# Optimization experiments

Measured on AMD Instinct MI355X. Metric: run time of the kernel, lower is better.

The kernel has to match this reference:

```python
import jax, jax.numpy as jnp
import numpy as np
from jax import lax

TAG_NUM = 20
START = TAG_NUM - 2  # tag2idx[START_TAG]
STOP = TAG_NUM - 1   # tag2idx[STOP_TAG]
NEG = -10000.0


def setup_inputs() -> dict:
    key = jax.random.key(0)
    k1, k2, k3, k4 = jax.random.split(key, 4)
    B, L = 256, 512
    feats = jax.random.normal(k1, (B, L, TAG_NUM), dtype=jnp.float32)
    T = jax.random.normal(k2, (TAG_NUM, TAG_NUM), dtype=jnp.float32)
    # transitions into START and out of... match torch init: T[START, :] = -1e4 ; T[:, STOP] = -1e4
    T = T.at[START, :].set(NEG).at[:, STOP].set(NEG)
    tags = jax.random.randint(k3, (B, L), 0, TAG_NUM - 2, dtype=jnp.int64)  # real tags only
    lengths = jax.random.randint(k4, (B,), 1, L + 1, dtype=jnp.int64)
    return {"feats": feats, "T": T, "tags": tags, "lengths": lengths}


def crf_neg_log_likelihood(feats, T, tags, lengths):
    # feats: [B, L, tag], T: [tag, tag] (T[i, j] = score of transition i -> j)
    B, L, tg = feats.shape
    mask = jnp.arange(L)[None, :] < lengths[:, None]           # [B, L] bool
    # scores[b, l, prev, cur] = feats[b, l, cur] + T[prev, cur]
    scores = feats[:, :, None, :] + T[None, None, :, :]        # [B, L, tag, tag]
    scores_lb = jnp.swapaxes(scores, 0, 1)                     # [L, B, tag, tag]
    mask_lb = mask.T                                           # [L, B]

    # ---- forward algorithm (log partition) ----
    part0 = scores_lb[0, :, START, :]                          # [B, tag]
    def step(part, x):
        sc, m = x                                              # sc: [B, tag, tag], m: [B]
        cur = jax.nn.logsumexp(sc + part[:, :, None], axis=1)  # [B, tag]
        part = jnp.where(m[:, None], cur, part)                # freeze past seq end
        return part, None
    part, _ = lax.scan(step, part0, (scores_lb[1:], mask_lb[1:]))
    final = jax.nn.logsumexp(part[:, :, None] + T[None, :, :], axis=1)  # [B, tag]
    forward_score = final[:, STOP].sum()

    # ---- gold score ----
    prev = jnp.concatenate([jnp.full((B, 1), START, dtype=tags.dtype), tags[:, :-1]], axis=1)
    b_idx = jnp.arange(B)[:, None]
    l_idx = jnp.arange(L)[None, :]
    tg_energy = scores[b_idx, l_idx, prev, tags]               # [B, L]
    gold = jnp.sum(tg_energy * mask.astype(feats.dtype))
    end_ids = jnp.take_along_axis(tags, lengths[:, None] - 1, axis=1)[:, 0]
    gold = gold + T[end_ids, STOP].sum()

    return forward_score - gold


def reference(feats, T, tags, lengths):
    return crf_neg_log_likelihood(feats, T, tags, lengths)
```

## Files before the change

### kernel.cpp

```cpp
#include <hip/hip_runtime.h>
#include <hip/hip_bf16.h>
#include <math.h>

#define TAGS   20
#define TSTART (TAGS - 2)
#define TSTOP  (TAGS - 1)

constexpr float  LOG2E = 1.4426950408889634f;
constexpr float  LN2f  = 0.6931471805599453f;
constexpr double LN2d  = 0.69314718055994530942;

typedef __attribute__((ext_vector_type(8))) short short8;
typedef __attribute__((ext_vector_type(4))) float f32x4;
union U4 { unsigned int u[4]; short8 v; };

__device__ __forceinline__ unsigned int pk2(float lo, float hi) {
    unsigned int a = __float_as_uint(hi) + 0x8000u;
    unsigned int b = __float_as_uint(lo) + 0x8000u;
#if __has_builtin(__builtin_amdgcn_perm)
    return __builtin_amdgcn_perm(a, b, 0x07060302u);
#else
    return (a & 0xFFFF0000u) | (b >> 16);
#endif
}
__device__ __forceinline__ float fexp2(float x) { return exp2f(x); }
__device__ __forceinline__ float flog2(float x) { return log2f(x); }
__device__ __forceinline__ float frcp(float x) { return __builtin_amdgcn_rcpf(x); }
__device__ __forceinline__ float bcast(float v, int srclane) {
    return __int_as_float(__builtin_amdgcn_readlane(__float_as_int(v), srclane));
}
__device__ __forceinline__ int rho(int k) {
    int g = k >> 3, i = k & 7;
    return (i < 4) ? (4 * g + i) : (16 + 4 * g + (i - 4));
}

__global__ __launch_bounds__(512)
void crf_fused_kernel(const float* __restrict__ feats,
                      const float* __restrict__ Tm,
                      const int*   __restrict__ tags,
                      const int*   __restrict__ lengths,
                      double*      __restrict__ partial,
                      int L)
{
    __shared__ float  smem[16 * 1024];
    __shared__ float  sv[32];
    __shared__ int    EsX[8];
    __shared__ float  gred[8];
    __shared__ double fwd_sh;

    const int b    = blockIdx.x;
    const int tid  = threadIdx.x;
    const int w    = tid >> 6;
    const int lane = tid & 63;
    const int G    = lane >> 4, col = lane & 15;
    const int len  = lengths[b];

    #pragma unroll
    for (int s = 0; s < 2; ++s) {
        const int c = w + 8 * s;
        float* efc = smem + c * 1024;
        const float* fc = feats + ((size_t)b * L + (size_t)c * 32) * TAGS;
        for (int it = lane; it < 160; it += 64) {
            float4 v = reinterpret_cast<const float4*>(fc)[it];
            float vv[4] = {v.x, v.y, v.z, v.w};
            #pragma unroll
            for (int u = 0; u < 4; ++u) {
                int f = it * 4 + u;
                int t = f / TAGS, tag = f - t * TAGS;
                efc[t * 32 + tag] = fexp2(vv[u] * LOG2E);
            }
        }
        for (int q = lane; q < 32 * 12; q += 64) {
            int t = q / 12;
            efc[t * 32 + 20 + (q - t * 12)] = 0.f;
        }
    }
    __syncthreads();

    U4 A0, A1;
    #pragma unroll
    for (int t = 0; t < 4; ++t) {
        int k0 = 8 * G + 2 * t;
        int r0 = rho(k0), r1 = rho(k0 + 1);
        int m1 = 16 + col;
        float a00 = (r0 < TAGS) ? fexp2(Tm[col * TAGS + r0] * LOG2E) : 0.f;
        float a01 = (r1 < TAGS) ? fexp2(Tm[col * TAGS + r1] * LOG2E) : 0.f;
        float a10 = (m1 < TAGS && r0 < TAGS) ? fexp2(Tm[m1 * TAGS + r0] * LOG2E) : 0.f;
        float a11 = (m1 < TAGS && r1 < TAGS) ? fexp2(Tm[m1 * TAGS + r1] * LOG2E) : 0.f;
        A0.u[t] = pk2(a00, a01);
        A1.u[t] = pk2(a10, a11);
    }

    auto step = [&](f32x4& C00, f32x4& C01, f32x4& C10, f32x4& C11,
                    const float* efc, int t) {
        float4 e0 = *reinterpret_cast<const float4*>(&efc[t * 32 + 4 * G]);
        float4 e1 = *reinterpret_cast<const float4*>(&efc[t * 32 + 16 + 4 * G]);
        U4 B0, B1;
        B0.u[0] = pk2(C00[0] * e0.x, C00[1] * e0.y);
        B0.u[1] = pk2(C00[2] * e0.z, C00[3] * e0.w);
        B0.u[2] = pk2(C10[0] * e1.x, C10[1] * e1.y);
        B0.u[3] = pk2(C10[2] * e1.z, C10[3] * e1.w);
        B1.u[0] = pk2(C01[0] * e0.x, C01[1] * e0.y);
        B1.u[1] = pk2(C01[2] * e0.z, C01[3] * e0.w);
        B1.u[2] = pk2(C11[0] * e1.x, C11[1] * e1.y);
        B1.u[3] = pk2(C11[2] * e1.z, C11[3] * e1.w);
        f32x4 z = {0.f, 0.f, 0.f, 0.f};
        C00 = __builtin_amdgcn_mfma_f32_16x16x32_bf16(A0.v, B0.v, z, 0, 0, 0);
        C01 = __builtin_amdgcn_mfma_f32_16x16x32_bf16(A0.v, B1.v, z, 0, 0, 0);
        C10 = __builtin_amdgcn_mfma_f32_16x16x32_bf16(A1.v, B0.v, z, 0, 0, 0);
        C11 = __builtin_amdgcn_mfma_f32_16x16x32_bf16(A1.v, B1.v, z, 0, 0, 0);
    };
    auto strip = [&](f32x4& C00, f32x4& C01, f32x4& C10, f32x4& C11) -> int {
        float pr = C00[0] + C00[1] + C00[2] + C00[3] + C10[0] + C10[1] + C10[2] + C10[3];
        int pb = __builtin_amdgcn_readfirstlane(__float_as_int(pr));
        int ex = ((pb >> 23) & 0xFF) - 127;
        float s = __uint_as_float((unsigned)(127 - ex) << 23);
        #pragma unroll
        for (int j = 0; j < 4; ++j) { C00[j] *= s; C01[j] *= s; C10[j] *= s; C11[j] *= s; }
        return ex;
    };
    auto xwr = [&](int slot, const f32x4& C00, const f32x4& C01,
                   const f32x4& C10, const f32x4& C11, int E) {
        float* Xs = smem + slot * 1088;
        #pragma unroll
        for (int j = 0; j < 4; ++j) {
            Xs[(4 * G + j) * 34 + col]           = C00[j];
            Xs[(4 * G + j) * 34 + col + 16]      = C01[j];
            Xs[(16 + 4 * G + j) * 34 + col]      = C10[j];
            Xs[(16 + 4 * G + j) * 34 + col + 16] = C11[j];
        }
        if (lane == 0) EsX[slot] = E;
    };
    auto prod = [&](int slot, f32x4& C00, f32x4& C01, f32x4& C10, f32x4& C11) -> int {
        const float* Xs = smem + slot * 1088;
        U4 Ax0, Ax1;
        #pragma unroll
        for (int t = 0; t < 4; ++t) {
            int r = rho(8 * G + 2 * t);
            float2 x0 = *reinterpret_cast<const float2*>(&Xs[col * 34 + r]);
            float2 x1 = *reinterpret_cast<const float2*>(&Xs[(16 + col) * 34 + r]);
            Ax0.u[t] = pk2(x0.x, x0.y);
            Ax1.u[t] = pk2(x1.x, x1.y);
        }
        U4 B0, B1;
        B0.u[0] = pk2(C00[0], C00[1]);
        B0.u[1] = pk2(C00[2], C00[3]);
        B0.u[2] = pk2(C10[0], C10[1]);
        B0.u[3] = pk2(C10[2], C10[3]);
        B1.u[0] = pk2(C01[0], C01[1]);
        B1.u[1] = pk2(C01[2], C01[3]);
        B1.u[2] = pk2(C11[0], C11[1]);
        B1.u[3] = pk2(C11[2], C11[3]);
        f32x4 z = {0.f, 0.f, 0.f, 0.f};
        f32x4 n00 = __builtin_amdgcn_mfma_f32_16x16x32_bf16(Ax0.v, B0.v, z, 0, 0, 0);
        f32x4 n01 = __builtin_amdgcn_mfma_f32_16x16x32_bf16(Ax0.v, B1.v, z, 0, 0, 0);
        f32x4 n10 = __builtin_amdgcn_mfma_f32_16x16x32_bf16(Ax1.v, B0.v, z, 0, 0, 0);
        f32x4 n11 = __builtin_amdgcn_mfma_f32_16x16x32_bf16(Ax1.v, B1.v, z, 0, 0, 0);
        C00 = n00; C01 = n01; C10 = n10; C11 = n11;
        return strip(C00, C01, C10, C11);
    };

    f32x4 aC00, aC01, aC10, aC11, bC00, bC01, bC10, bC11;
    #pragma unroll
    for (int j = 0; j < 4; ++j) {
        float d = (4 * G + j == col) ? 1.f : 0.f;
        aC00[j] = d; aC11[j] = d; aC01[j] = 0.f; aC10[j] = 0.f;
        bC00[j] = d; bC11[j] = d; bC01[j] = 0.f; bC10[j] = 0.f;
    }
    int aE = 0, bE = 0;

    const int cB  = w + 8;
    const int loA = (w == 0) ? 1 : w * 32;
    const int hiA = min(w * 32 + 31, len - 1);
    const int loB = cB * 32;
    const int hiB = min(cB * 32 + 31, len - 1);
    int nA = hiA - loA + 1; if (nA < 0) nA = 0;
    int nB = hiB - loB + 1; if (nB < 0) nB = 0;
    const int n = max(nA, nB);
    const float* efA = smem + w * 1024;
    const float* efB = smem + cB * 1024;

    int lA = hiA, lB = hiB;
    for (int i = 0; i < n; ++i) {
        if (i < nA) { step(aC00, aC01, aC10, aC11, efA, lA - w * 32);  --lA; }
        if (i < nB) { step(bC00, bC01, bC10, bC11, efB, lB - cB * 32); --lB; }
        if ((i & 3) == 3) {
            aE += strip(aC00, aC01, aC10, aC11);
            bE += strip(bC00, bC01, bC10, bC11);
        }
    }
    __syncthreads();

    if ((w & 1) == 0) {
        xwr(w / 2,     aC00, aC01, aC10, aC11, aE);
        xwr(w / 2 + 4, bC00, bC01, bC10, bC11, bE);
    }
    __syncthreads();
    if (w & 1) {
        int pA = (w - 1) / 2;
        aE += EsX[pA]     + prod(pA,     aC00, aC01, aC10, aC11);
        bE += EsX[pA + 4] + prod(pA + 4, bC00, bC01, bC10, bC11);
    }
    __syncthreads();
    if (w == 1 || w == 5) {
        xwr((w - 1) / 4,     aC00, aC01, aC10, aC11, aE);
        xwr((w - 1) / 4 + 2, bC00, bC01, bC10, bC11, bE);
    }
    __syncthreads();
    if (w == 3 || w == 7) {
        int q = (w - 3) / 4;
        aE += EsX[q]     + prod(q,     aC00, aC01, aC10, aC11);
        bE += EsX[q + 2] + prod(q + 2, bC00, bC01, bC10, bC11);
    }
    __syncthreads();
    if (w == 3) {
        xwr(0, aC00, aC01, aC10, aC11, aE);
        xwr(1, bC00, bC01, bC10, bC11, bE);
    }
    __syncthreads();
    if (w == 7) {
        aE += EsX[0] + prod(0, aC00, aC01, aC10, aC11);
        bE += EsX[1] + prod(1, bC00, bC01, bC10, bC11);
    }
    __syncthreads();
    if (w == 7) {
        xwr(0, aC00, aC01, aC10, aC11, aE);
        int ex = prod(0, bC00, bC01, bC10, bC11);
        int fE = aE + bE + ex;
        float* Gt = smem;
        #pragma unroll
        for (int j = 0; j < 4; ++j) {
            Gt[col * 34 + 4 * G + j]            = bC00[j];
            Gt[col * 34 + 16 + 4 * G + j]       = bC10[j];
            Gt[(col + 16) * 34 + 4 * G + j]     = bC01[j];
            Gt[(col + 16) * 34 + 16 + 4 * G + j]= bC11[j];
        }
        if (lane == 0) EsX[0] = fE;
    }
    __syncthreads();

    if (w == 0) {
        const int n2 = lane & 31;
        float p = (n2 < TAGS) ? (feats[(size_t)b * L * TAGS + n2] + Tm[TSTART * TAGS + n2]) * LOG2E
                              : -1e30f;
        float mx = p;
        #pragma unroll
        for (int off = 32; off; off >>= 1) mx = fmaxf(mx, __shfl_xor(mx, off));
        float v = (n2 < TAGS) ? fexp2(p - mx) : 0.f;
        if (lane < 32) sv[lane] = v;
        const float* Gt = smem;
        float vn = 0.f;
        #pragma unroll
        for (int r = 0; r < 32; r += 2) {
            float2 g2 = *reinterpret_cast<const float2*>(&Gt[n2 * 34 + r]);
            vn = fmaf(sv[r], g2.x, vn);
            vn = fmaf(sv[r + 1], g2.y, vn);
        }
        float cstop = Tm[n2 * TAGS + TSTOP];
        float mc = (n2 < TAGS) ? cstop : -INFINITY;
        #pragma unroll
        for (int off = 32; off; off >>= 1) mc = fmaxf(mc, __shfl_xor(mc, off));
        float ts = (lane < 32 && n2 < TAGS) ? vn * fexp2((cstop - mc) * LOG2E) : 0.f;
        #pragma unroll
        for (int off = 32; off; off >>= 1) ts += __shfl_xor(ts, off);
        if (lane == 0)
            fwd_sh = ((double)mx + (double)EsX[0] + (double)flog2(ts)) * LN2d + (double)mc;
    }

    float g = 0.f;
    for (int l = tid; l < len; l += 512) {
        int tt = tags[(size_t)b * L + l];
        int pv = (l == 0) ? TSTART : tags[(size_t)b * L + l - 1];
        g += feats[((size_t)b * L + l) * TAGS + tt] + Tm[pv * TAGS + tt];
    }
    #pragma unroll
    for (int off = 32; off; off >>= 1) g += __shfl_xor(g, off);
    if (lane == 0) gred[w] = g;
    __syncthreads();

    if (tid == 0) {
        float gs = gred[0] + gred[1] + gred[2] + gred[3]
                 + gred[4] + gred[5] + gred[6] + gred[7];
        double gold = (double)gs + (double)Tm[tags[(size_t)b * L + len - 1] * TAGS + TSTOP];
        partial[b] = fwd_sh - gold;
    }
}

__global__ __launch_bounds__(64)
void crf_fwd_kernel(const float* __restrict__ feats,
                    const float* __restrict__ Tm,
                    const int*   __restrict__ tags,
                    const int*   __restrict__ lengths,
                    double*      __restrict__ partial,
                    int B, int L)
{
    __shared__ float le[512 * TAGS];
    const int b    = blockIdx.x;
    const int lane = threadIdx.x;
    const int j    = (lane < TAGS) ? lane : 0;
    const float* fb  = feats + (size_t)b * L * TAGS;
    const int*   tg  = tags  + (size_t)b * L;
    const int    len = lengths[b];

    const int nv4 = (L * TAGS) >> 2;
    for (int it = lane; it < nv4; it += 64) {
        float4 v = reinterpret_cast<const float4*>(fb)[it];
        float4 e;
        e.x = fexp2(v.x * LOG2E); e.y = fexp2(v.y * LOG2E);
        e.z = fexp2(v.z * LOG2E); e.w = fexp2(v.w * LOG2E);
        reinterpret_cast<float4*>(le)[it] = e;
    }
    __syncthreads();

    float ET[TAGS];
    #pragma unroll
    for (int i = 0; i < TAGS; ++i) ET[i] = fexp2(Tm[i * TAGS + j] * LOG2E);

    float w0   = flog2(le[j]) + Tm[TSTART * TAGS + j] * LOG2E;
    float base = bcast(w0, 0);
    float P    = fexp2(w0 - base);
    float M2   = base;
    float Pa[TAGS];
    #pragma unroll
    for (int i = 0; i < TAGS; ++i) Pa[i] = bcast(P, i);
    const float* leb = le + j;

    auto STEP = [&](int l, float efv, float rsv, bool scaled) {
        float s0 = 0.f, s1 = 0.f, s2 = 0.f, s3 = 0.f;
        #pragma unroll
        for (int i = 0; i < TAGS; i += 4) {
            s0 = fmaf(ET[i + 0], Pa[i + 0], s0);
            s1 = fmaf(ET[i + 1], Pa[i + 1], s1);
            s2 = fmaf(ET[i + 2], Pa[i + 2], s2);
            s3 = fmaf(ET[i + 3], Pa[i + 3], s3);
        }
        float s   = (s0 + s1) + (s2 + s3);
        float cur = s * efv;
        float pn  = (l < len) ? cur : P;
        P = scaled ? pn * rsv : pn;
        #pragma unroll
        for (int i = 0; i < TAGS; ++i) Pa[i] = bcast(P, i);
    };

    float efb[4];
    #pragma unroll
    for (int k = 0; k < 4; ++k) { int ln = 1 + k; ln = (ln < L) ? ln : (L - 1); efb[k] = leb[ln * TAGS]; }

    float rs = 1.0f, lg0 = 0.0f;
    int l0 = 1;
    for (; l0 + 3 < L; l0 += 4) {
        if (l0 >= len) break;
        float efn[4];
        #pragma unroll
        for (int k = 0; k < 4; ++k) { int ln = l0 + 4 + k; ln = (ln < L) ? ln : (L - 1); efn[k] = leb[ln * TAGS]; }
        M2 += lg0;
        STEP(l0 + 0, efb[0], rs, true);
        STEP(l0 + 1, efb[1], 1.f, false);
        STEP(l0 + 2, efb[2], 1.f, false);
        STEP(l0 + 3, efb[3], 1.f, false);
        float p0 = Pa[0];
        rs = frcp(p0); lg0 = flog2(p0);
        #pragma unroll
        for (int k = 0; k < 4; ++k) efb[k] = efn[k];
    }
    if (l0 < len) {
        int rem = L - l0;
        M2 += lg0;
        if (rem > 0) STEP(l0 + 0, efb[0], rs, true);
        if (rem > 1) STEP(l0 + 1, efb[1], 1.f, false);
        if (rem > 2) STEP(l0 + 2, efb[2], 1.f, false);
        if (rem > 3) STEP(l0 + 3, efb[3], 1.f, false);
    }

    float cstop = Tm[j * TAGS + TSTOP];
    float mc = (lane < TAGS) ? cstop : -INFINITY;
    #pragma unroll
    for (int off = 32; off; off >>= 1) mc = fmaxf(mc, __shfl_xor(mc, off));
    float t = (lane < TAGS) ? P * fexp2((cstop - mc) * LOG2E) : 0.f;
    #pragma unroll
    for (int off = 32; off; off >>= 1) t += __shfl_xor(t, off);
    double fwd = ((double)M2 + (double)flog2(t)) * LN2d + (double)mc;

    float g = 0.f;
    for (int l = lane; l < len; l += 64) {
        int tt = tg[l];
        int pv = (l == 0) ? TSTART : tg[l - 1];
        g += flog2(le[l * TAGS + tt]) * LN2f + Tm[pv * TAGS + tt];
    }
    #pragma unroll
    for (int off = 32; off; off >>= 1) g += __shfl_xor(g, off);

    if (lane == 0) {
        double gold = (double)g + (double)Tm[tg[len - 1] * TAGS + TSTOP];
        partial[b] = fwd - gold;
    }
}

__global__ __launch_bounds__(256)
void crf_reduce_kernel(const double* __restrict__ partial, float* __restrict__ out, int B)
{
    __shared__ double sh[256];
    const int t = threadIdx.x;
    double acc = 0.0;
    for (int i = t; i < B; i += 256) acc += partial[i];
    sh[t] = acc;
    __syncthreads();
    for (int s = 128; s; s >>= 1) {
        if (t < s) sh[t] += sh[t + s];
        __syncthreads();
    }
    if (t == 0) out[0] = (float)sh[0];
}

extern "C" void kernel_launch(void* const* d_in, const int* in_sizes, int n_in,
                              void* d_out, int out_size, void* d_ws, size_t ws_size,
                              hipStream_t stream)
{
    const float* feats   = (const float*)d_in[0];
    const float* Tm      = (const float*)d_in[1];
    const int*   tags    = (const int*)d_in[2];
    const int*   lengths = (const int*)d_in[3];

    const int B = in_sizes[3];
    const int L = in_sizes[2] / B;

    double* partial = (double*)d_ws;

    if (L == 512 && ws_size >= (size_t)B * sizeof(double)) {
        crf_fused_kernel<<<B, 512, 0, stream>>>(feats, Tm, tags, lengths, partial, L);
        crf_reduce_kernel<<<1, 256, 0, stream>>>(partial, (float*)d_out, B);
    } else {
        crf_fwd_kernel<<<B, 64, 0, stream>>>(feats, Tm, tags, lengths, partial, B, L);
        crf_reduce_kernel<<<1, 256, 0, stream>>>(partial, (float*)d_out, B);
    }
}
```

Measured before the change: 28.87 us.

## Use 16 waves per batch row and fuse final reduction via atomics

Raises the fused kernel to 1024 threads so each of 16 waves handles one 32-step chunk of the sequence, instead of 8 waves each interleaving two chunks. The tree combine of chunk transfer matrices grows to four levels. The separate reduce kernel is replaced by a fixed-point 64-bit atomic accumulation with a last-block-done counter, plus a memset launch. Hardware exp2/log builtins are also used. This halves the serial MFMA chain per wave but lowers occupancy per CU and adds combine barriers.

```diff
diff --git a/kernel.cpp b/kernel.cpp
--- a/kernel.cpp
+++ b/kernel.cpp
@@ -23,8 +23,16 @@
     return (a & 0xFFFF0000u) | (b >> 16);
 #endif
 }
+#if __has_builtin(__builtin_amdgcn_exp2f)
+__device__ __forceinline__ float fexp2(float x) { return __builtin_amdgcn_exp2f(x); }
+#else
 __device__ __forceinline__ float fexp2(float x) { return exp2f(x); }
+#endif
+#if __has_builtin(__builtin_amdgcn_logf)
+__device__ __forceinline__ float flog2(float x) { return __builtin_amdgcn_logf(x); }
+#else
 __device__ __forceinline__ float flog2(float x) { return log2f(x); }
+#endif
 __device__ __forceinline__ float frcp(float x) { return __builtin_amdgcn_rcpf(x); }
 __device__ __forceinline__ float bcast(float v, int srclane) {
     return __int_as_float(__builtin_amdgcn_readlane(__float_as_int(v), srclane));
@@ -34,18 +42,20 @@
     return (i < 4) ? (4 * g + i) : (16 + 4 * g + (i - 4));
 }
 
-__global__ __launch_bounds__(512)
+__global__ __launch_bounds__(1024)
 void crf_fused_kernel(const float* __restrict__ feats,
                       const float* __restrict__ Tm,
                       const int*   __restrict__ tags,
                       const int*   __restrict__ lengths,
-                      double*      __restrict__ partial,
+                      unsigned long long* __restrict__ acc,
+                      unsigned int*       __restrict__ cnt,
+                      float*              __restrict__ out,
                       int L)
 {
     __shared__ float  smem[16 * 1024];
     __shared__ float  sv[32];
     __shared__ int    EsX[8];
-    __shared__ float  gred[8];
+    __shared__ float  gred[16];
     __shared__ double fwd_sh;
 
     const int b    = blockIdx.x;
@@ -55,27 +65,22 @@
     const int G    = lane >> 4, col = lane & 15;
     const int len  = lengths[b];
 
-    #pragma unroll
-    for (int s = 0; s < 2; ++s) {
-        const int c = w + 8 * s;
-        float* efc = smem + c * 1024;
-        const float* fc = feats + ((size_t)b * L + (size_t)c * 32) * TAGS;
-        for (int it = lane; it < 160; it += 64) {
-            float4 v = reinterpret_cast<const float4*>(fc)[it];
-            float vv[4] = {v.x, v.y, v.z, v.w};
-            #pragma unroll
-            for (int u = 0; u < 4; ++u) {
-                int f = it * 4 + u;
-                int t = f / TAGS, tag = f - t * TAGS;
-                efc[t * 32 + tag] = fexp2(vv[u] * LOG2E);
-            }
-        }
-        for (int q = lane; q < 32 * 12; q += 64) {
-            int t = q / 12;
-            efc[t * 32 + 20 + (q - t * 12)] = 0.f;
-        }
-    }
-    __syncthreads();
+    float* efc = smem + w * 1024;
+    const float* fc = feats + ((size_t)b * L + (size_t)w * 32) * TAGS;
+    for (int it = lane; it < 160; it += 64) {
+        float4 v = reinterpret_cast<const float4*>(fc)[it];
+        float vv[4] = {v.x, v.y, v.z, v.w};
+        #pragma unroll
+        for (int u = 0; u < 4; ++u) {
+            int f = it * 4 + u;
+            int t = f / TAGS, tag = f - t * TAGS;
+            efc[t * 32 + tag] = fexp2(vv[u] * LOG2E);
+        }
+    }
+    for (int q = lane; q < 32 * 12; q += 64) {
+        int t = q / 12;
+        efc[t * 32 + 20 + (q - t * 12)] = 0.f;
+    }
 
     U4 A0, A1;
     #pragma unroll
@@ -91,25 +96,6 @@
         A1.u[t] = pk2(a10, a11);
     }
 
-    auto step = [&](f32x4& C00, f32x4& C01, f32x4& C10, f32x4& C11,
-                    const float* efc, int t) {
-        float4 e0 = *reinterpret_cast<const float4*>(&efc[t * 32 + 4 * G]);
-        float4 e1 = *reinterpret_cast<const float4*>(&efc[t * 32 + 16 + 4 * G]);
-        U4 B0, B1;
-        B0.u[0] = pk2(C00[0] * e0.x, C00[1] * e0.y);
-        B0.u[1] = pk2(C00[2] * e0.z, C00[3] * e0.w);
-        B0.u[2] = pk2(C10[0] * e1.x, C10[1] * e1.y);
-        B0.u[3] = pk2(C10[2] * e1.z, C10[3] * e1.w);
-        B1.u[0] = pk2(C01[0] * e0.x, C01[1] * e0.y);
-        B1.u[1] = pk2(C01[2] * e0.z, C01[3] * e0.w);
-        B1.u[2] = pk2(C11[0] * e1.x, C11[1] * e1.y);
-        B1.u[3] = pk2(C11[2] * e1.z, C11[3] * e1.w);
-        f32x4 z = {0.f, 0.f, 0.f, 0.f};
-        C00 = __builtin_amdgcn_mfma_f32_16x16x32_bf16(A0.v, B0.v, z, 0, 0, 0);
-        C01 = __builtin_amdgcn_mfma_f32_16x16x32_bf16(A0.v, B1.v, z, 0, 0, 0);
-        C10 = __builtin_amdgcn_mfma_f32_16x16x32_bf16(A1.v, B0.v, z, 0, 0, 0);
-        C11 = __builtin_amdgcn_mfma_f32_16x16x32_bf16(A1.v, B1.v, z, 0, 0, 0);
-    };
     auto strip = [&](f32x4& C00, f32x4& C01, f32x4& C10, f32x4& C11) -> int {
         float pr = C00[0] + C00[1] + C00[2] + C00[3] + C10[0] + C10[1] + C10[2] + C10[3];
         int pb = __builtin_amdgcn_readfirstlane(__float_as_int(pr));
@@ -160,82 +146,63 @@
         return strip(C00, C01, C10, C11);
     };
 
-    f32x4 aC00, aC01, aC10, aC11, bC00, bC01, bC10, bC11;
+    f32x4 C00, C01, C10, C11;
     #pragma unroll
     for (int j = 0; j < 4; ++j) {
         float d = (4 * G + j == col) ? 1.f : 0.f;
-        aC00[j] = d; aC11[j] = d; aC01[j] = 0.f; aC10[j] = 0.f;
-        bC00[j] = d; bC11[j] = d; bC01[j] = 0.f; bC10[j] = 0.f;
-    }
-    int aE = 0, bE = 0;
-
-    const int cB  = w + 8;
-    const int loA = (w == 0) ? 1 : w * 32;
-    const int hiA = min(w * 32 + 31, len - 1);
-    const int loB = cB * 32;
-    const int hiB = min(cB * 32 + 31, len - 1);
-    int nA = hiA - loA + 1; if (nA < 0) nA = 0;
-    int nB = hiB - loB + 1; if (nB < 0) nB = 0;
-    const int n = max(nA, nB);
-    const float* efA = smem + w * 1024;
-    const float* efB = smem + cB * 1024;
-
-    int lA = hiA, lB = hiB;
-    for (int i = 0; i < n; ++i) {
-        if (i < nA) { step(aC00, aC01, aC10, aC11, efA, lA - w * 32);  --lA; }
-        if (i < nB) { step(bC00, bC01, bC10, bC11, efB, lB - cB * 32); --lB; }
-        if ((i & 3) == 3) {
-            aE += strip(aC00, aC01, aC10, aC11);
-            bE += strip(bC00, bC01, bC10, bC11);
-        }
-    }
-    __syncthreads();
-
-    if ((w & 1) == 0) {
-        xwr(w / 2,     aC00, aC01, aC10, aC11, aE);
-        xwr(w / 2 + 4, bC00, bC01, bC10, bC11, bE);
-    }
-    __syncthreads();
-    if (w & 1) {
-        int pA = (w - 1) / 2;
-        aE += EsX[pA]     + prod(pA,     aC00, aC01, aC10, aC11);
-        bE += EsX[pA + 4] + prod(pA + 4, bC00, bC01, bC10, bC11);
-    }
-    __syncthreads();
-    if (w == 1 || w == 5) {
-        xwr((w - 1) / 4,     aC00, aC01, aC10, aC11, aE);
-        xwr((w - 1) / 4 + 2, bC00, bC01, bC10, bC11, bE);
-    }
-    __syncthreads();
-    if (w == 3 || w == 7) {
-        int q = (w - 3) / 4;
-        aE += EsX[q]     + prod(q,     aC00, aC01, aC10, aC11);
-        bE += EsX[q + 2] + prod(q + 2, bC00, bC01, bC10, bC11);
-    }
-    __syncthreads();
-    if (w == 3) {
-        xwr(0, aC00, aC01, aC10, aC11, aE);
-        xwr(1, bC00, bC01, bC10, bC11, bE);
-    }
-    __syncthreads();
-    if (w == 7) {
-        aE += EsX[0] + prod(0, aC00, aC01, aC10, aC11);
-        bE += EsX[1] + prod(1, bC00, bC01, bC10, bC11);
-    }
-    __syncthreads();
-    if (w == 7) {
-        xwr(0, aC00, aC01, aC10, aC11, aE);
-        int ex = prod(0, bC00, bC01, bC10, bC11);
-        int fE = aE + bE + ex;
+        C00[j] = d; C11[j] = d; C01[j] = 0.f; C10[j] = 0.f;
+    }
+    int E = 0;
+
+    const int lo  = (w == 0) ? 1 : w * 32;
+    const int hiE = min(w * 32 + 31, len - 1);
+    for (int l = hiE; l >= lo; --l) {
+        const int t = l - w * 32;
+        float4 e0 = *reinterpret_cast<const float4*>(&efc[t * 32 + 4 * G]);
+        float4 e1 = *reinterpret_cast<const float4*>(&efc[t * 32 + 16 + 4 * G]);
+        U4 B0, B1;
+        B0.u[0] = pk2(C00[0] * e0.x, C00[1] * e0.y);
+        B0.u[1] = pk2(C00[2] * e0.z, C00[3] * e0.w);
+        B0.u[2] = pk2(C10[0] * e1.x, C10[1] * e1.y);
+        B0.u[3] = pk2(C10[2] * e1.z, C10[3] * e1.w);
+        B1.u[0] = pk2(C01[0] * e0.x, C01[1] * e0.y);
+        B1.u[1] = pk2(C01[2] * e0.z, C01[3] * e0.w);
+        B1.u[2] = pk2(C11[0] * e1.x, C11[1] * e1.y);
+        B1.u[3] = pk2(C11[2] * e1.z, C11[3] * e1.w);
+        f32x4 z = {0.f, 0.f, 0.f, 0.f};
+        C00 = __builtin_amdgcn_mfma_f32_16x16x32_bf16(A0.v, B0.v, z, 0, 0, 0);
+        C01 = __builtin_amdgcn_mfma_f32_16x16x32_bf16(A0.v, B1.v, z, 0, 0, 0);
+        C10 = __builtin_amdgcn_mfma_f32_16x16x32_bf16(A1.v, B0.v, z, 0, 0, 0);
+        C11 = __builtin_amdgcn_mfma_f32_16x16x32_bf16(A1.v, B1.v, z, 0, 0, 0);
+        if ((l & 3) == 0) E += strip(C00, C01, C10, C11);
+    }
+    __syncthreads();
+
+    if ((w & 1) == 0) xwr(w >> 1, C00, C01, C10, C11, E);
+    __syncthreads();
+    if (w & 1) { int s = (w - 1) >> 1; E += EsX[s] + prod(s, C00, C01, C10, C11); }
+    __syncthreads();
+    if ((w & 3) == 1) xwr((w - 1) >> 2, C00, C01, C10, C11, E);
+    __syncthreads();
+    if ((w & 3) == 3) { int s = (w - 3) >> 2; E += EsX[s] + prod(s, C00, C01, C10, C11); }
+    __syncthreads();
+    if ((w & 7) == 3) xwr((w - 3) >> 3, C00, C01, C10, C11, E);
+    __syncthreads();
+    if ((w & 7) == 7) { int s = (w - 7) >> 3; E += EsX[s] + prod(s, C00, C01, C10, C11); }
+    __syncthreads();
+    if (w == 7) xwr(0, C00, C01, C10, C11, E);
+    __syncthreads();
+    if (w == 15) {
+        E += EsX[0] + prod(0, C00, C01, C10, C11);
         float* Gt = smem;
         #pragma unroll
         for (int j = 0; j < 4; ++j) {
-            Gt[col * 34 + 4 * G + j]            = bC00[j];
-            Gt[col * 34 + 16 + 4 * G + j]       = bC10[j];
-            Gt[(col + 16) * 34 + 4 * G + j]     = bC01[j];
-            Gt[(col + 16) * 34 + 16 + 4 * G + j]= bC11[j];
-        }
-        if (lane == 0) EsX[0] = fE;
+            Gt[col * 34 + 4 * G + j]             = C00[j];
+            Gt[col * 34 + 16 + 4 * G + j]        = C10[j];
+            Gt[(col + 16) * 34 + 4 * G + j]      = C01[j];
+            Gt[(col + 16) * 34 + 16 + 4 * G + j] = C11[j];
+        }
+        if (lane == 0) EsX[0] = E;
     }
     __syncthreads();
 
@@ -268,7 +235,7 @@
     }
 
     float g = 0.f;
-    for (int l = tid; l < len; l += 512) {
+    for (int l = tid; l < len; l += 1024) {
         int tt = tags[(size_t)b * L + l];
         int pv = (l == 0) ? TSTART : tags[(size_t)b * L + l - 1];
         g += feats[((size_t)b * L + l) * TAGS + tt] + Tm[pv * TAGS + tt];
@@ -279,10 +246,19 @@
     __syncthreads();
 
     if (tid == 0) {
-        float gs = gred[0] + gred[1] + gred[2] + gred[3]
-                 + gred[4] + gred[5] + gred[6] + gred[7];
+        float gs = 0.f;
+        #pragma unroll
+        for (int i = 0; i < 16; ++i) gs += gred[i];
         double gold = (double)gs + (double)Tm[tags[(size_t)b * L + len - 1] * TAGS + TSTOP];
-        partial[b] = fwd_sh - gold;
+        double pd   = fwd_sh - gold;
+        long long q = (long long)(pd * 1048576.0 + (pd >= 0.0 ? 0.5 : -0.5));
+        atomicAdd(acc, (unsigned long long)q);
+        __threadfence();
+        unsigned int c = atomicAdd(cnt, 1u);
+        if (c == gridDim.x - 1) {
+            long long tot = (long long)atomicAdd(acc, 0ULL);
+            out[0] = (float)((double)tot * (1.0 / 1048576.0));
+        }
     }
 }
 
@@ -424,12 +400,14 @@
     const int B = in_sizes[3];
     const int L = in_sizes[2] / B;
 
-    double* partial = (double*)d_ws;
-
-    if (L == 512 && ws_size >= (size_t)B * sizeof(double)) {
-        crf_fused_kernel<<<B, 512, 0, stream>>>(feats, Tm, tags, lengths, partial, L);
-        crf_reduce_kernel<<<1, 256, 0, stream>>>(partial, (float*)d_out, B);
+    if (L == 512 && ws_size >= 64) {
+        unsigned long long* acc = (unsigned long long*)d_ws;
+        unsigned int*       cnt = (unsigned int*)((char*)d_ws + 8);
+        hipMemsetAsync(d_ws, 0, 64, stream);
+        crf_fused_kernel<<<B, 1024, 0, stream>>>(feats, Tm, tags, lengths,
+                                                 acc, cnt, (float*)d_out, L);
     } else {
+        double* partial = (double*)((char*)d_ws + 64);
         crf_fwd_kernel<<<B, 64, 0, stream>>>(feats, Tm, tags, lengths, partial, B, L);
         crf_reduce_kernel<<<1, 256, 0, stream>>>(partial, (float*)d_out, B);
     }
```

Result: slower. 30.64 us (+6.1%).

## Fold emission and rescale into per-step A operand; renormalize every step lazily

Applied to the files above, without the earlier changes.

Instead of scaling the carried C matrix by emission exponentials before packing, the per-step A operand is rebuilt as exp(T)*exp(feat)*scale, so C is packed directly. The exponent stripping moves into every step and the scale is applied lazily through the A operand rather than by multiplying all sixteen C registers every fourth step. exp2/log2 are also switched to the raw AMDGCN hardware builtins. This adds per-step A packing and a readfirstlane reduction on the serial chain, in exchange for dropping the separate strip passes.

```diff
diff --git a/kernel.cpp b/kernel.cpp
--- a/kernel.cpp
+++ b/kernel.cpp
@@ -23,8 +23,16 @@
     return (a & 0xFFFF0000u) | (b >> 16);
 #endif
 }
+#if __has_builtin(__builtin_amdgcn_exp2f)
+__device__ __forceinline__ float fexp2(float x) { return __builtin_amdgcn_exp2f(x); }
+#else
 __device__ __forceinline__ float fexp2(float x) { return exp2f(x); }
+#endif
+#if __has_builtin(__builtin_amdgcn_logf)
+__device__ __forceinline__ float flog2(float x) { return __builtin_amdgcn_logf(x); }
+#else
 __device__ __forceinline__ float flog2(float x) { return log2f(x); }
+#endif
 __device__ __forceinline__ float frcp(float x) { return __builtin_amdgcn_rcpf(x); }
 __device__ __forceinline__ float bcast(float v, int srclane) {
     return __int_as_float(__builtin_amdgcn_readlane(__float_as_int(v), srclane));
@@ -77,39 +85,51 @@
     }
     __syncthreads();
 
-    U4 A0, A1;
-    #pragma unroll
-    for (int t = 0; t < 4; ++t) {
-        int k0 = 8 * G + 2 * t;
-        int r0 = rho(k0), r1 = rho(k0 + 1);
+    float ET0[8], ET1[8];
+    #pragma unroll
+    for (int e = 0; e < 8; ++e) {
+        int r  = rho(8 * G + e);
         int m1 = 16 + col;
-        float a00 = (r0 < TAGS) ? fexp2(Tm[col * TAGS + r0] * LOG2E) : 0.f;
-        float a01 = (r1 < TAGS) ? fexp2(Tm[col * TAGS + r1] * LOG2E) : 0.f;
-        float a10 = (m1 < TAGS && r0 < TAGS) ? fexp2(Tm[m1 * TAGS + r0] * LOG2E) : 0.f;
-        float a11 = (m1 < TAGS && r1 < TAGS) ? fexp2(Tm[m1 * TAGS + r1] * LOG2E) : 0.f;
-        A0.u[t] = pk2(a00, a01);
-        A1.u[t] = pk2(a10, a11);
+        ET0[e] = (r < TAGS) ? fexp2(Tm[col * TAGS + r] * LOG2E) : 0.f;
+        ET1[e] = (m1 < TAGS && r < TAGS) ? fexp2(Tm[m1 * TAGS + r] * LOG2E) : 0.f;
     }
 
     auto step = [&](f32x4& C00, f32x4& C01, f32x4& C10, f32x4& C11,
-                    const float* efc, int t) {
+                    float& s, int& E, const float* efc, int t) {
         float4 e0 = *reinterpret_cast<const float4*>(&efc[t * 32 + 4 * G]);
         float4 e1 = *reinterpret_cast<const float4*>(&efc[t * 32 + 16 + 4 * G]);
+        float f0 = s * e0.x, f1 = s * e0.y, f2 = s * e0.z, f3 = s * e0.w;
+        float f4 = s * e1.x, f5 = s * e1.y, f6 = s * e1.z, f7 = s * e1.w;
+        U4 Al0, Al1;
+        Al0.u[0] = pk2(ET0[0] * f0, ET0[1] * f1);
+        Al0.u[1] = pk2(ET0[2] * f2, ET0[3] * f3);
+        Al0.u[2] = pk2(ET0[4] * f4, ET0[5] * f5);
+        Al0.u[3] = pk2(ET0[6] * f6, ET0[7] * f7);
+        Al1.u[0] = pk2(ET1[0] * f0, ET1[1] * f1);
+        Al1.u[1] = pk2(ET1[2] * f2, ET1[3] * f3);
+        Al1.u[2] = pk2(ET1[4] * f4, ET1[5] * f5);
+        Al1.u[3] = pk2(ET1[6] * f6, ET1[7] * f7);
         U4 B0, B1;
-        B0.u[0] = pk2(C00[0] * e0.x, C00[1] * e0.y);
-        B0.u[1] = pk2(C00[2] * e0.z, C00[3] * e0.w);
-        B0.u[2] = pk2(C10[0] * e1.x, C10[1] * e1.y);
-        B0.u[3] = pk2(C10[2] * e1.z, C10[3] * e1.w);
-        B1.u[0] = pk2(C01[0] * e0.x, C01[1] * e0.y);
-        B1.u[1] = pk2(C01[2] * e0.z, C01[3] * e0.w);
-        B1.u[2] = pk2(C11[0] * e1.x, C11[1] * e1.y);
-        B1.u[3] = pk2(C11[2] * e1.z, C11[3] * e1.w);
+        B0.u[0] = pk2(C00[0], C00[1]);
+        B0.u[1] = pk2(C00[2], C00[3]);
+        B0.u[2] = pk2(C10[0], C10[1]);
+        B0.u[3] = pk2(C10[2], C10[3]);
+        B1.u[0] = pk2(C01[0], C01[1]);
+        B1.u[1] = pk2(C01[2], C01[3]);
+        B1.u[2] = pk2(C11[0], C11[1]);
+        B1.u[3] = pk2(C11[2], C11[3]);
         f32x4 z = {0.f, 0.f, 0.f, 0.f};
-        C00 = __builtin_amdgcn_mfma_f32_16x16x32_bf16(A0.v, B0.v, z, 0, 0, 0);
-        C01 = __builtin_amdgcn_mfma_f32_16x16x32_bf16(A0.v, B1.v, z, 0, 0, 0);
-        C10 = __builtin_amdgcn_mfma_f32_16x16x32_bf16(A1.v, B0.v, z, 0, 0, 0);
-        C11 = __builtin_amdgcn_mfma_f32_16x16x32_bf16(A1.v, B1.v, z, 0, 0, 0);
+        C00 = __builtin_amdgcn_mfma_f32_16x16x32_bf16(Al0.v, B0.v, z, 0, 0, 0);
+        C01 = __builtin_amdgcn_mfma_f32_16x16x32_bf16(Al0.v, B1.v, z, 0, 0, 0);
+        C10 = __builtin_amdgcn_mfma_f32_16x16x32_bf16(Al1.v, B0.v, z, 0, 0, 0);
+        C11 = __builtin_amdgcn_mfma_f32_16x16x32_bf16(Al1.v, B1.v, z, 0, 0, 0);
+        float pr = C00[0] + C00[1] + C00[2] + C00[3] + C10[0] + C10[1] + C10[2] + C10[3];
+        int pb = __builtin_amdgcn_readfirstlane(__float_as_int(pr));
+        int ex = ((pb >> 23) & 0xFF) - 127;
+        s = __uint_as_float((unsigned)(127 - ex) << 23);
+        E += ex;
     };
+
     auto strip = [&](f32x4& C00, f32x4& C01, f32x4& C10, f32x4& C11) -> int {
         float pr = C00[0] + C00[1] + C00[2] + C00[3] + C10[0] + C10[1] + C10[2] + C10[3];
         int pb = __builtin_amdgcn_readfirstlane(__float_as_int(pr));
@@ -167,7 +187,8 @@
         aC00[j] = d; aC11[j] = d; aC01[j] = 0.f; aC10[j] = 0.f;
         bC00[j] = d; bC11[j] = d; bC01[j] = 0.f; bC10[j] = 0.f;
     }
-    int aE = 0, bE = 0;
+    int   aE = 0,   bE = 0;
+    float sA = 1.f, sB = 1.f;
 
     const int cB  = w + 8;
     const int loA = (w == 0) ? 1 : w * 32;
@@ -182,12 +203,13 @@
 
     int lA = hiA, lB = hiB;
     for (int i = 0; i < n; ++i) {
-        if (i < nA) { step(aC00, aC01, aC10, aC11, efA, lA - w * 32);  --lA; }
-        if (i < nB) { step(bC00, bC01, bC10, bC11, efB, lB - cB * 32); --lB; }
-        if ((i & 3) == 3) {
-            aE += strip(aC00, aC01, aC10, aC11);
-            bE += strip(bC00, bC01, bC10, bC11);
-        }
+        if (i < nA) { step(aC00, aC01, aC10, aC11, sA, aE, efA, lA - w * 32);  --lA; }
+        if (i < nB) { step(bC00, bC01, bC10, bC11, sB, bE, efB, lB - cB * 32); --lB; }
+    }
+    #pragma unroll
+    for (int j = 0; j < 4; ++j) {
+        aC00[j] *= sA; aC01[j] *= sA; aC10[j] *= sA; aC11[j] *= sA;
+        bC00[j] *= sB; bC01[j] *= sB; bC10[j] *= sB; bC11[j] *= sB;
     }
     __syncthreads();
 
```

Result: slower. 36.06 us (+24.9%).

## Split each wave's sequence chunk into two independent half-chains for MFMA ILP

Applied to the files above, without the earlier changes.

Each wave now runs four independent 16-step transfer-matrix product chains instead of two 32-step chains. This halves the serial dependency length and interleaves more independent MFMAs. The two halves are combined at the end with an in-wave shared-memory matrix product, adding one extra product and one more barrier. The block barrier after the exp preload is removed because each wave only reads the chunks it wrote itself. exp2/log2 are also switched to the raw amdgcn intrinsics, which may reduce accuracy slightly.

```diff
diff --git a/kernel.cpp b/kernel.cpp
--- a/kernel.cpp
+++ b/kernel.cpp
@@ -23,8 +23,16 @@
     return (a & 0xFFFF0000u) | (b >> 16);
 #endif
 }
+#if __has_builtin(__builtin_amdgcn_exp2f)
+__device__ __forceinline__ float fexp2(float x) { return __builtin_amdgcn_exp2f(x); }
+#else
 __device__ __forceinline__ float fexp2(float x) { return exp2f(x); }
+#endif
+#if __has_builtin(__builtin_amdgcn_logf)
+__device__ __forceinline__ float flog2(float x) { return __builtin_amdgcn_logf(x); }
+#else
 __device__ __forceinline__ float flog2(float x) { return log2f(x); }
+#endif
 __device__ __forceinline__ float frcp(float x) { return __builtin_amdgcn_rcpf(x); }
 __device__ __forceinline__ float bcast(float v, int srclane) {
     return __int_as_float(__builtin_amdgcn_readlane(__float_as_int(v), srclane));
@@ -75,7 +83,6 @@
             efc[t * 32 + 20 + (q - t * 12)] = 0.f;
         }
     }
-    __syncthreads();
 
     U4 A0, A1;
     #pragma unroll
@@ -119,9 +126,8 @@
         for (int j = 0; j < 4; ++j) { C00[j] *= s; C01[j] *= s; C10[j] *= s; C11[j] *= s; }
         return ex;
     };
-    auto xwr = [&](int slot, const f32x4& C00, const f32x4& C01,
-                   const f32x4& C10, const f32x4& C11, int E) {
-        float* Xs = smem + slot * 1088;
+    auto xwrP = [&](float* Xs, const f32x4& C00, const f32x4& C01,
+                    const f32x4& C10, const f32x4& C11) {
         #pragma unroll
         for (int j = 0; j < 4; ++j) {
             Xs[(4 * G + j) * 34 + col]           = C00[j];
@@ -129,10 +135,9 @@
             Xs[(16 + 4 * G + j) * 34 + col]      = C10[j];
             Xs[(16 + 4 * G + j) * 34 + col + 16] = C11[j];
         }
-        if (lane == 0) EsX[slot] = E;
-    };
-    auto prod = [&](int slot, f32x4& C00, f32x4& C01, f32x4& C10, f32x4& C11) -> int {
-        const float* Xs = smem + slot * 1088;
+    };
+    auto prodP = [&](const float* Xs, f32x4& C00, f32x4& C01,
+                     f32x4& C10, f32x4& C11) -> int {
         U4 Ax0, Ax1;
         #pragma unroll
         for (int t = 0; t < 4; ++t) {
@@ -159,108 +164,134 @@
         C00 = n00; C01 = n01; C10 = n10; C11 = n11;
         return strip(C00, C01, C10, C11);
     };
-
-    f32x4 aC00, aC01, aC10, aC11, bC00, bC01, bC10, bC11;
+    auto xwr = [&](int slot, const f32x4& C00, const f32x4& C01,
+                   const f32x4& C10, const f32x4& C11, int E) {
+        xwrP(smem + slot * 1088, C00, C01, C10, C11);
+        if (lane == 0) EsX[slot] = E;
+    };
+    auto prod = [&](int slot, f32x4& C00, f32x4& C01, f32x4& C10, f32x4& C11) -> int {
+        return prodP(smem + slot * 1088, C00, C01, C10, C11);
+    };
+
+    f32x4 C0_00, C0_01, C0_10, C0_11, C1_00, C1_01, C1_10, C1_11;
+    f32x4 C2_00, C2_01, C2_10, C2_11, C3_00, C3_01, C3_10, C3_11;
     #pragma unroll
     for (int j = 0; j < 4; ++j) {
         float d = (4 * G + j == col) ? 1.f : 0.f;
-        aC00[j] = d; aC11[j] = d; aC01[j] = 0.f; aC10[j] = 0.f;
-        bC00[j] = d; bC11[j] = d; bC01[j] = 0.f; bC10[j] = 0.f;
-    }
-    int aE = 0, bE = 0;
-
-    const int cB  = w + 8;
-    const int loA = (w == 0) ? 1 : w * 32;
-    const int hiA = min(w * 32 + 31, len - 1);
-    const int loB = cB * 32;
-    const int hiB = min(cB * 32 + 31, len - 1);
-    int nA = hiA - loA + 1; if (nA < 0) nA = 0;
-    int nB = hiB - loB + 1; if (nB < 0) nB = 0;
-    const int n = max(nA, nB);
+        C0_00[j] = d; C0_11[j] = d; C0_01[j] = 0.f; C0_10[j] = 0.f;
+        C1_00[j] = d; C1_11[j] = d; C1_01[j] = 0.f; C1_10[j] = 0.f;
+        C2_00[j] = d; C2_11[j] = d; C2_01[j] = 0.f; C2_10[j] = 0.f;
+        C3_00[j] = d; C3_11[j] = d; C3_01[j] = 0.f; C3_10[j] = 0.f;
+    }
+    int E0 = 0, E1 = 0, E2 = 0, E3 = 0;
+
+    const int baseA = w * 32, baseB = (w + 8) * 32;
+    const int lo0 = (w == 0) ? 1 : baseA;
+    const int hi0 = min(baseA + 15, len - 1);
+    const int lo1 = baseA + 16;
+    const int hi1 = min(baseA + 31, len - 1);
+    const int lo2 = baseB;
+    const int hi2 = min(baseB + 15, len - 1);
+    const int lo3 = baseB + 16;
+    const int hi3 = min(baseB + 31, len - 1);
+    int n0 = max(hi0 - lo0 + 1, 0), n1 = max(hi1 - lo1 + 1, 0);
+    int n2 = max(hi2 - lo2 + 1, 0), n3 = max(hi3 - lo3 + 1, 0);
+    const int nmax = max(max(n0, n1), max(n2, n3));
     const float* efA = smem + w * 1024;
-    const float* efB = smem + cB * 1024;
-
-    int lA = hiA, lB = hiB;
-    for (int i = 0; i < n; ++i) {
-        if (i < nA) { step(aC00, aC01, aC10, aC11, efA, lA - w * 32);  --lA; }
-        if (i < nB) { step(bC00, bC01, bC10, bC11, efB, lB - cB * 32); --lB; }
+    const float* efB = smem + (w + 8) * 1024;
+
+    int l0 = hi0, l1 = hi1, l2 = hi2, l3 = hi3;
+    for (int i = 0; i < nmax; ++i) {
+        if (i < n0) { step(C0_00, C0_01, C0_10, C0_11, efA, l0 - baseA); --l0; }
+        if (i < n1) { step(C1_00, C1_01, C1_10, C1_11, efA, l1 - baseA); --l1; }
+        if (i < n2) { step(C2_00, C2_01, C2_10, C2_11, efB, l2 - baseB); --l2; }
+        if (i < n3) { step(C3_00, C3_01, C3_10, C3_11, efB, l3 - baseB); --l3; }
         if ((i & 3) == 3) {
-            aE += strip(aC00, aC01, aC10, aC11);
-            bE += strip(bC00, bC01, bC10, bC11);
-        }
-    }
+            E0 += strip(C0_00, C0_01, C0_10, C0_11);
+            E1 += strip(C1_00, C1_01, C1_10, C1_11);
+            E2 += strip(C2_00, C2_01, C2_10, C2_11);
+            E3 += strip(C3_00, C3_01, C3_10, C3_11);
+        }
+    }
+    __syncthreads();
+
+    float* myslot = smem + w * 1088;
+    xwrP(myslot, C0_00, C0_01, C0_10, C0_11);
+    int aE = E0 + E1 + prodP(myslot, C1_00, C1_01, C1_10, C1_11);
+    xwrP(myslot, C2_00, C2_01, C2_10, C2_11);
+    int bE = E2 + E3 + prodP(myslot, C3_00, C3_01, C3_10, C3_11);
     __syncthreads();
 
     if ((w & 1) == 0) {
-        xwr(w / 2,     aC00, aC01, aC10, aC11, aE);
-        xwr(w / 2 + 4, bC00, bC01, bC10, bC11, bE);
+        xwr(w / 2,     C1_00, C1_01, C1_10, C1_11, aE);
+        xwr(w / 2 + 4, C3_00, C3_01, C3_10, C3_11, bE);
     }
     __syncthreads();
     if (w & 1) {
         int pA = (w - 1) / 2;
-        aE += EsX[pA]     + prod(pA,     aC00, aC01, aC10, aC11);
-        bE += EsX[pA + 4] + prod(pA + 4, bC00, bC01, bC10, bC11);
+        aE += EsX[pA]     + prod(pA,     C1_00, C1_01, C1_10, C1_11);
+        bE += EsX[pA + 4] + prod(pA + 4, C3_00, C3_01, C3_10, C3_11);
     }
     __syncthreads();
     if (w == 1 || w == 5) {
-        xwr((w - 1) / 4,     aC00, aC01, aC10, aC11, aE);
-        xwr((w - 1) / 4 + 2, bC00, bC01, bC10, bC11, bE);
+        xwr((w - 1) / 4,     C1_00, C1_01, C1_10, C1_11, aE);
+        xwr((w - 1) / 4 + 2, C3_00, C3_01, C3_10, C3_11, bE);
     }
     __syncthreads();
     if (w == 3 || w == 7) {
         int q = (w - 3) / 4;
-        aE += EsX[q]     + prod(q,     aC00, aC01, aC10, aC11);
-        bE += EsX[q + 2] + prod(q + 2, bC00, bC01, bC10, bC11);
+        aE += EsX[q]     + prod(q,     C1_00, C1_01, C1_10, C1_11);
+        bE += EsX[q + 2] + prod(q + 2, C3_00, C3_01, C3_10, C3_11);
     }
     __syncthreads();
     if (w == 3) {
-        xwr(0, aC00, aC01, aC10, aC11, aE);
-        xwr(1, bC00, bC01, bC10, bC11, bE);
+        xwr(0, C1_00, C1_01, C1_10, C1_11, aE);
+        xwr(1, C3_00, C3_01, C3_10, C3_11, bE);
     }
     __syncthreads();
     if (w == 7) {
-        aE += EsX[0] + prod(0, aC00, aC01, aC10, aC11);
-        bE += EsX[1] + prod(1, bC00, bC01, bC10, bC11);
+        aE += EsX[0] + prod(0, C1_00, C1_01, C1_10, C1_11);
+        bE += EsX[1] + prod(1, C3_00, C3_01, C3_10, C3_11);
     }
     __syncthreads();
     if (w == 7) {
-        xwr(0, aC00, aC01, aC10, aC11, aE);
-        int ex = prod(0, bC00, bC01, bC10, bC11);
+        xwr(0, C1_00, C1_01, C1_10, C1_11, aE);
+        int ex = prod(0, C3_00, C3_01, C3_10, C3_11);
         int fE = aE + bE + ex;
         float* Gt = smem;
         #pragma unroll
         for (int j = 0; j < 4; ++j) {
-            Gt[col * 34 + 4 * G + j]            = bC00[j];
-            Gt[col * 34 + 16 + 4 * G + j]       = bC10[j];
-            Gt[(col + 16) * 34 + 4 * G + j]     = bC01[j];
-            Gt[(col + 16) * 34 + 16 + 4 * G + j]= bC11[j];
+            Gt[col * 34 + 4 * G + j]             = C3_00[j];
+            Gt[col * 34 + 16 + 4 * G + j]        = C3_10[j];
+            Gt[(col + 16) * 34 + 4 * G + j]      = C3_01[j];
+            Gt[(col + 16) * 34 + 16 + 4 * G + j] = C3_11[j];
         }
         if (lane == 0) EsX[0] = fE;
     }
     __syncthreads();
 
     if (w == 0) {
-        const int n2 = lane & 31;
-        float p = (n2 < TAGS) ? (feats[(size_t)b * L * TAGS + n2] + Tm[TSTART * TAGS + n2]) * LOG2E
-                              : -1e30f;
+        const int n2_ = lane & 31;
+        float p = (n2_ < TAGS) ? (feats[(size_t)b * L * TAGS + n2_] + Tm[TSTART * TAGS + n2_]) * LOG2E
+                               : -1e30f;
         float mx = p;
         #pragma unroll
         for (int off = 32; off; off >>= 1) mx = fmaxf(mx, __shfl_xor(mx, off));
-        float v = (n2 < TAGS) ? fexp2(p - mx) : 0.f;
+        float v = (n2_ < TAGS) ? fexp2(p - mx) : 0.f;
         if (lane < 32) sv[lane] = v;
         const float* Gt = smem;
         float vn = 0.f;
         #pragma unroll
         for (int r = 0; r < 32; r += 2) {
-            float2 g2 = *reinterpret_cast<const float2*>(&Gt[n2 * 34 + r]);
+            float2 g2 = *reinterpret_cast<const float2*>(&Gt[n2_ * 34 + r]);
             vn = fmaf(sv[r], g2.x, vn);
             vn = fmaf(sv[r + 1], g2.y, vn);
         }
-        float cstop = Tm[n2 * TAGS + TSTOP];
-        float mc = (n2 < TAGS) ? cstop : -INFINITY;
+        float cstop = Tm[n2_ * TAGS + TSTOP];
+        float mc = (n2_ < TAGS) ? cstop : -INFINITY;
         #pragma unroll
         for (int off = 32; off; off >>= 1) mc = fmaxf(mc, __shfl_xor(mc, off));
-        float ts = (lane < 32 && n2 < TAGS) ? vn * fexp2((cstop - mc) * LOG2E) : 0.f;
+        float ts = (lane < 32 && n2_ < TAGS) ? vn * fexp2((cstop - mc) * LOG2E) : 0.f;
         #pragma unroll
         for (int off = 32; off; off >>= 1) ts += __shfl_xor(ts, off);
         if (lane == 0)
```

New measurement: 29.69 us. 1.03x slower.
